# Performance work log

Hardware: AMD Instinct MI355X
Metric: run time of the kernel (lower is better)

Reference implementation:

```python
import jax, jax.numpy as jnp
import numpy as np

B, S, D_IN, D_OUT, H = 2, 2048, 1024, 1024, 16
HD = D_OUT // H  # head dim = 64


def setup_inputs() -> dict:
    key = jax.random.key(0)
    ks = jax.random.split(key, 9)
    s_in = 1.0 / np.sqrt(D_IN)
    s_out = 1.0 / np.sqrt(D_OUT)
    return {
        "X": jax.random.normal(ks[0], (B, S, D_IN), dtype=jnp.float32),
        "Wq": jax.random.uniform(ks[1], (D_OUT, D_IN), jnp.float32, -s_in, s_in),
        "bq": jax.random.uniform(ks[2], (D_OUT,), jnp.float32, -s_in, s_in),
        "Wk": jax.random.uniform(ks[3], (D_OUT, D_IN), jnp.float32, -s_in, s_in),
        "bk": jax.random.uniform(ks[4], (D_OUT,), jnp.float32, -s_in, s_in),
        "Wv": jax.random.uniform(ks[5], (D_OUT, D_IN), jnp.float32, -s_in, s_in),
        "bv": jax.random.uniform(ks[6], (D_OUT,), jnp.float32, -s_in, s_in),
        "Wo": jax.random.uniform(ks[7], (D_OUT, D_OUT), jnp.float32, -s_out, s_out),
        "bo": jax.random.uniform(ks[8], (D_OUT,), jnp.float32, -s_out, s_out),
    }


def reference(X, Wq, bq, Wk, bk, Wv, bv, Wo, bo):
    scale = jnp.asarray(HD ** 0.5, X.dtype)  # self.dim = sqrt(head_dim)
    q = X @ Wq.T + bq  # [B,S,D_OUT]
    k = X @ Wk.T + bk
    v = X @ Wv.T + bv
    # split heads: b s (h d) -> b h s d
    q = q.reshape(B, S, H, HD).transpose(0, 2, 1, 3)
    k = k.reshape(B, S, H, HD).transpose(0, 2, 1, 3)
    v = v.reshape(B, S, H, HD).transpose(0, 2, 1, 3)
    scores = jnp.einsum('bhsd,bhtd->bhst', q, k) / scale  # [B,H,S,S]
    causal = jnp.triu(jnp.ones((S, S), dtype=bool), k=1)
    scores = jnp.where(causal, -jnp.inf, scores)
    weights = jax.nn.softmax(scores, axis=-1)
    out = jnp.einsum('bhst,bhtd->bhsd', weights, v)  # [B,H,S,HD]
    out = out.transpose(0, 2, 1, 3).reshape(B, S, D_OUT)  # b h s d -> b s (h d)
    return out @ Wo.T + bo
```

## Files before the change

### kernel.cpp

```cpp
#include <hip/hip_runtime.h>
#include <hip/hip_bf16.h>

typedef __bf16 bf16_t;
typedef __bf16 bf16x8 __attribute__((ext_vector_type(8)));
typedef float  f32x4  __attribute__((ext_vector_type(4)));
typedef unsigned short ushort_t;

#define MFMA16(a, b, c) __builtin_amdgcn_mfma_f32_16x16x32_bf16((a), (b), (c), 0, 0, 0)
#define GLDS16(g, l) __builtin_amdgcn_global_load_lds( \
    (const __attribute__((address_space(1))) unsigned int*)(g), \
    (__attribute__((address_space(3))) unsigned int*)(l), 16, 0, 0)

#define WAITCNT_VM(n)  (0x0F70 | (n))
#define WAITCNT_LGKM0  0xC07F

#define QSCALE 0.18033688f

__global__ __launch_bounds__(256) void cvt_all(
    const void* __restrict__ X,  const void* __restrict__ W0, const void* __restrict__ W1,
    const void* __restrict__ W2, const void* __restrict__ W3,
    const void* __restrict__ c0, const void* __restrict__ c1,
    const void* __restrict__ c2, const void* __restrict__ c3,
    bf16_t* __restrict__ Xb, bf16_t* __restrict__ Wb, float* __restrict__ biasF,
    int* __restrict__ flag)
{
    const int tid  = threadIdx.x;
    const int lane = tid & 63;
    const ushort_t u = ((const ushort_t*)X)[2 * lane];
    const int e = (u >> 7) & 0xFF;
    const int f = (__ballot(e >= 0xA0) != 0ull) ? 1 : 0;

    const int bid = blockIdx.x;
    if (bid >= 4096) {
        if (bid == 4096 && tid == 0) *flag = f;
        const int idx = ((bid - 4096) * 256 + tid) * 8;
        const int w = idx >> 10, off = idx & 1023;
        const void* src = (w == 0) ? c0 : (w == 1) ? c1 : (w == 2) ? c2 : c3;
        #pragma unroll
        for (int r = 0; r < 8; ++r)
            biasF[idx + r] = f ? ((const float*)src)[off + r]
                               : (float)((const bf16_t*)src)[off + r];
        return;
    }

    const long long i = (long long)bid * 2048 + tid * 8;
    const void* src;
    bf16_t* dst;
    long long off;
    if (i < 4194304) { src = X; dst = Xb; off = i; }
    else {
        const int w = (int)((i - 4194304) >> 20);
        off = (i - 4194304) & 1048575;
        src = (w == 0) ? W0 : (w == 1) ? W1 : (w == 2) ? W2 : W3;
        dst = Wb + (size_t)w * 1048576;
    }
    if (f) {
        const float* s = (const float*)src + off;
        const float4 a = *(const float4*)(s);
        const float4 b = *(const float4*)(s + 4);
        bf16x8 o;
        o[0] = (bf16_t)a.x; o[1] = (bf16_t)a.y; o[2] = (bf16_t)a.z; o[3] = (bf16_t)a.w;
        o[4] = (bf16_t)b.x; o[5] = (bf16_t)b.y; o[6] = (bf16_t)b.z; o[7] = (bf16_t)b.w;
        *(bf16x8*)(dst + off) = o;
    } else {
        *(bf16x8*)(dst + off) = *(const bf16x8*)((const bf16_t*)src + off);
    }
}

template<int TM>
__global__ __launch_bounds__(256, 2) void gemm_nt(
    const bf16_t* __restrict__ A,
    const bf16_t* __restrict__ W0, const bf16_t* __restrict__ W1, const bf16_t* __restrict__ W2,
    const float* __restrict__ b0, const float* __restrict__ b1, const float* __restrict__ b2,
    void* __restrict__ C, int ldc, bf16_t* __restrict__ Vt, int fuse_vt,
    const int* __restrict__ flag, int is_out)
{
    constexpr int MI = TM / 32;
    constexpr int G  = (TM == 128) ? 4 : 3;
    __shared__ bf16_t Ash[3][TM * 32];
    __shared__ bf16_t Bsh[3][128 * 32];

    const int f32out = is_out ? *flag : 0;

    const int tid  = threadIdx.x;
    const int wid  = tid >> 6;
    const int lane = tid & 63;
    const int g    = lane >> 4;
    const int c    = lane & 15;

    const int m0  = blockIdx.x * TM;
    const int n0  = blockIdx.y * 128;
    const int mat = n0 >> 10;
    const bf16_t* W  = (mat == 0) ? W0 : (mat == 1) ? W1 : W2;
    const float*  bs = (mat == 0) ? b0 : (mat == 1) ? b1 : b2;
    const int nw = n0 & 1023;

    const int srow = lane >> 2;
    const int sblk = (lane & 3) ^ ((lane >> 3) & 3);
    const bf16_t* Ag = A + (size_t)(m0 + wid * (TM / 4) + srow) * 1024 + sblk * 8;
    const bf16_t* Wg = W + (size_t)(nw + wid * 32 + srow) * 1024 + sblk * 8;

    const int waveM = (wid >> 1) * (TM / 2);
    const int waveN = (wid & 1) * 64;

    f32x4 acc[MI][4] = {};
    const int fblk = (g ^ ((c >> 1) & 3)) * 8;

    auto stage = [&](int t, int buf) {
        const int k0 = t * 32;
        bf16_t* As = &Ash[buf][(wid * (TM / 4)) * 32];
        bf16_t* Bs = &Bsh[buf][(wid * 32) * 32];
        GLDS16(Ag + k0, As);
        if (TM == 128) GLDS16(Ag + (size_t)16 * 1024 + k0, As + 16 * 32);
        GLDS16(Wg + k0, Bs);
        GLDS16(Wg + (size_t)16 * 1024 + k0, Bs + 16 * 32);
    };

    stage(0, 0);
    stage(1, 1);

    #pragma unroll 3
    for (int k = 0; k < 32; ++k) {
        if (k < 30) {
            stage(k + 2, (k + 2) % 3);
            __builtin_amdgcn_s_waitcnt(WAITCNT_VM(2 * G));
        } else if (k == 30) {
            __builtin_amdgcn_s_waitcnt(WAITCNT_VM(G));
        } else {
            __builtin_amdgcn_s_waitcnt(WAITCNT_VM(0));
        }
        __builtin_amdgcn_s_barrier();
        asm volatile("" ::: "memory");

        const int cur = k % 3;
        bf16x8 af[MI], bfr[4];
        #pragma unroll
        for (int i = 0; i < MI; ++i)
            af[i] = *(const bf16x8*)(&Ash[cur][(waveM + i * 16 + c) * 32 + fblk]);
        #pragma unroll
        for (int j = 0; j < 4; ++j)
            bfr[j] = *(const bf16x8*)(&Bsh[cur][(waveN + j * 16 + c) * 32 + fblk]);
        #pragma unroll
        for (int i = 0; i < MI; ++i)
            #pragma unroll
            for (int j = 0; j < 4; ++j)
                acc[i][j] = MFMA16(af[i], bfr[j], acc[i][j]);

        asm volatile("" ::: "memory");
        __builtin_amdgcn_s_waitcnt(WAITCNT_LGKM0);
        __builtin_amdgcn_s_barrier();
    }

    if (fuse_vt && mat == 2) {
        #pragma unroll
        for (int j = 0; j < 4; ++j) {
            const int col  = n0 + waveN + j * 16 + c;
            const int hcol = col & 1023;
            const float bv = bs[hcol];
            const int h = hcol >> 6, d = hcol & 63;
            #pragma unroll
            for (int i = 0; i < MI; ++i) {
                const int row = m0 + waveM + i * 16 + g * 4;
                const int bb = row >> 11, s = row & 2047;
                bf16_t pk[4];
                #pragma unroll
                for (int r = 0; r < 4; ++r) pk[r] = (bf16_t)(acc[i][j][r] + bv);
                *(uint2*)(&Vt[(((size_t)bb * 16 + h) * 64 + d) * 2048 + s]) = *(uint2*)pk;
            }
        }
        return;
    }

    const float oscale = (fuse_vt && mat == 0) ? QSCALE : 1.0f;
    #pragma unroll
    for (int j = 0; j < 4; ++j) {
        const int col = n0 + waveN + j * 16 + c;
        const float bv = bs[col & 1023];
        #pragma unroll
        for (int i = 0; i < MI; ++i) {
            const int row = m0 + waveM + i * 16 + g * 4;
            #pragma unroll
            for (int r = 0; r < 4; ++r) {
                const float val = (acc[i][j][r] + bv) * oscale;
                const size_t idx = (size_t)(row + r) * ldc + col;
                if (f32out) ((float*)C)[idx] = val;
                else        ((bf16_t*)C)[idx] = (bf16_t)val;
            }
        }
    }
}

__global__ __launch_bounds__(256, 4) void attn_kernel(
    const bf16_t* __restrict__ QKV, const bf16_t* __restrict__ Vt,
    bf16_t* __restrict__ O)
{
    __shared__ bf16_t Ksh[64][72];
    __shared__ bf16_t Vsh[64][72];
    __shared__ bf16_t Psh[4][16][72];

    const int tid  = threadIdx.x;
    const int wid  = tid >> 6;
    const int lane = tid & 63;
    const int g    = lane >> 4;
    const int c    = lane & 15;

    const int bh = blockIdx.y;
    const int b  = bh >> 4, h = bh & 15;
    const int qt = (bh < 16) ? blockIdx.x : (31 - blockIdx.x);
    const int q0 = qt * 64;
    const int nt = qt + 1;

    bf16x8 aq[2];
    {
        const bf16_t* qp = QKV + (size_t)(b * 2048 + q0 + wid * 16 + c) * 3072 + h * 64;
        aq[0] = *(const bf16x8*)(qp + g * 8);
        aq[1] = *(const bf16x8*)(qp + 32 + g * 8);
    }

    float li[4] = {};
    f32x4 o[4]  = {};

    const int sr  = tid >> 2;
    const int sc0 = (tid & 3) * 16;
    const bf16_t* Kg = QKV + (size_t)(b * 2048 + sr) * 3072 + 1024 + h * 64 + sc0;
    const bf16_t* Vg = Vt + ((size_t)bh * 64 + sr) * 2048 + sc0;

    uint4 kr0 = *(const uint4*)(Kg);
    uint4 kr1 = *(const uint4*)(Kg + 8);
    uint4 vr0 = *(const uint4*)(Vg);
    uint4 vr1 = *(const uint4*)(Vg + 8);

    for (int jt = 0; jt < nt; ++jt) {
        *(uint4*)(&Ksh[sr][sc0])     = kr0;
        *(uint4*)(&Ksh[sr][sc0 + 8]) = kr1;
        *(uint4*)(&Vsh[sr][sc0])     = vr0;
        *(uint4*)(&Vsh[sr][sc0 + 8]) = vr1;
        __syncthreads();

        if (jt + 1 < nt) {
            const size_t ko = (size_t)(jt + 1) * 64 * 3072;
            kr0 = *(const uint4*)(Kg + ko);
            kr1 = *(const uint4*)(Kg + ko + 8);
            vr0 = *(const uint4*)(Vg + (jt + 1) * 64);
            vr1 = *(const uint4*)(Vg + (jt + 1) * 64 + 8);
        }

        f32x4 s[4] = {};
        #pragma unroll
        for (int n = 0; n < 4; ++n)
            #pragma unroll
            for (int kb = 0; kb < 2; ++kb) {
                const bf16x8 kf = *(const bf16x8*)(&Ksh[n * 16 + c][kb * 32 + g * 8]);
                s[n] = MFMA16(aq[kb], kf, s[n]);
            }

        if (jt == nt - 1) {
            const int j0 = jt * 64;
            const int qrow = q0 + wid * 16 + g * 4;
            #pragma unroll
            for (int n = 0; n < 4; ++n)
                #pragma unroll
                for (int r = 0; r < 4; ++r)
                    if (j0 + n * 16 + c > qrow + r) s[n][r] = -1e30f;
        }

        #pragma unroll
        for (int n = 0; n < 4; ++n)
            #pragma unroll
            for (int r = 0; r < 4; ++r) {
                const float p = __builtin_amdgcn_exp2f(s[n][r]);
                li[r] += p;
                Psh[wid][g * 4 + r][n * 16 + c] = (bf16_t)p;
            }
        __builtin_amdgcn_wave_barrier();

        #pragma unroll
        for (int kb = 0; kb < 2; ++kb) {
            const bf16x8 ap = *(const bf16x8*)(&Psh[wid][c][kb * 32 + g * 8]);
            #pragma unroll
            for (int d = 0; d < 4; ++d) {
                const bf16x8 vf = *(const bf16x8*)(&Vsh[d * 16 + c][kb * 32 + g * 8]);
                o[d] = MFMA16(ap, vf, o[d]);
            }
        }
        __syncthreads();
    }

    #pragma unroll
    for (int off = 1; off < 16; off <<= 1)
        #pragma unroll
        for (int r = 0; r < 4; ++r)
            li[r] += __shfl_xor(li[r], off, 64);

    const int orow = b * 2048 + q0 + wid * 16 + g * 4;
    #pragma unroll
    for (int r = 0; r < 4; ++r) {
        const float inv = 1.0f / li[r];
        #pragma unroll
        for (int d = 0; d < 4; ++d)
            O[(size_t)(orow + r) * 1024 + h * 64 + d * 16 + c] = (bf16_t)(o[d][r] * inv);
    }
}

extern "C" void kernel_launch(void* const* d_in, const int* in_sizes, int n_in,
                              void* d_out, int out_size, void* d_ws, size_t ws_size,
                              hipStream_t stream)
{
    const void* X  = d_in[0];
    const void* Wq = d_in[1];  const void* bq = d_in[2];
    const void* Wk = d_in[3];  const void* bk = d_in[4];
    const void* Wv = d_in[5];  const void* bv = d_in[6];
    const void* Wo = d_in[7];  const void* bo = d_in[8];

    int*    flag  = (int*)d_ws;
    float*  biasF = (float*)((char*)d_ws + 16);
    bf16_t* Xb    = (bf16_t*)((char*)d_ws + 16 + 16384);
    bf16_t* Wb    = Xb  + (size_t)4096 * 1024;
    bf16_t* QKV   = Wb  + (size_t)4 * 1024 * 1024;
    bf16_t* Vt    = QKV + (size_t)4096 * 3072;
    bf16_t* Ao    = Vt  + (size_t)4096 * 1024;

    const size_t MW = (size_t)1024 * 1024;

    cvt_all<<<4098, 256, 0, stream>>>(X, Wq, Wk, Wv, Wo, bq, bk, bv, bo,
                                      Xb, Wb, biasF, flag);

    gemm_nt<128><<<dim3(32, 24), 256, 0, stream>>>(
        Xb, Wb, Wb + MW, Wb + 2 * MW,
        biasF, biasF + 1024, biasF + 2048, QKV, 3072, Vt, 1, flag, 0);
    attn_kernel<<<dim3(32, 32), 256, 0, stream>>>(QKV, Vt, Ao);
    gemm_nt<64><<<dim3(64, 8), 256, 0, stream>>>(
        Ao, Wb + 3 * MW, Wb + 3 * MW, Wb + 3 * MW,
        biasF + 3072, biasF + 3072, biasF + 3072, d_out, 1024, (bf16_t*)nullptr, 0, flag, 1);
}
```

Baseline: 201.1 us.

## Add 256x256-tile, 8-wave QKV projection GEMM with 4-stage LDS pipeline

Replaces the 128x128-tile QKV projection GEMM with a new 512-thread kernel that computes 256x256 output tiles. It uses a four-buffer direct global-to-LDS prefetch ring with split half-phase MFMA blocks, barriers and raised wave priority. Larger tiles raise arithmetic intensity and cut global traffic per FLOP. The trade-offs are a grid of only 192 blocks on a 256-CU device, much more LDS (128KB) and a large register footprint. The epilogue keeps the Q scaling and the transposed V store.

```diff
diff --git a/kernel.cpp b/kernel.cpp
--- a/kernel.cpp
+++ b/kernel.cpp
@@ -13,6 +13,8 @@
 
 #define WAITCNT_VM(n)  (0x0F70 | (n))
 #define WAITCNT_LGKM0  0xC07F
+
+#define MEMFENCE asm volatile("" ::: "memory")
 
 #define QSCALE 0.18033688f
 
@@ -67,6 +69,141 @@
     }
 }
 
+__global__ __launch_bounds__(512, 2) void gemm256(
+    const bf16_t* __restrict__ A,
+    const bf16_t* __restrict__ W0, const bf16_t* __restrict__ W1, const bf16_t* __restrict__ W2,
+    const float* __restrict__ b0, const float* __restrict__ b1, const float* __restrict__ b2,
+    bf16_t* __restrict__ C, bf16_t* __restrict__ Vt)
+{
+    __shared__ bf16_t Ash[4][256 * 32];
+    __shared__ bf16_t Bsh[4][256 * 32];
+
+    const int tid  = threadIdx.x;
+    const int wid  = tid >> 6;
+    const int lane = tid & 63;
+    const int g    = lane >> 4;
+    const int c    = lane & 15;
+
+    const int m0  = blockIdx.x * 256;
+    const int n0  = blockIdx.y * 256;
+    const int mat = n0 >> 10;
+    const bf16_t* W  = (mat == 0) ? W0 : (mat == 1) ? W1 : W2;
+    const float*  bs = (mat == 0) ? b0 : (mat == 1) ? b1 : b2;
+    const int nw = n0 & 1023;
+
+    const int srow = lane >> 2;
+    const int sblk = (lane & 3) ^ ((lane >> 3) & 3);
+    const bf16_t* Ag = A + (size_t)(m0 + wid * 32 + srow) * 1024 + sblk * 8;
+    const bf16_t* Wg = W + (size_t)(nw + wid * 32 + srow) * 1024 + sblk * 8;
+
+    const int waveM = (wid >> 2) * 128;
+    const int waveN = (wid & 3) * 64;
+    const int fblk  = (g ^ ((c >> 1) & 3)) * 8;
+
+    f32x4 acc[8][4] = {};
+
+    auto stageA = [&](int H, int q) {
+        GLDS16(Ag + (size_t)(q * 16) * 1024 + H * 32, &Ash[H & 3][(wid * 32 + q * 16) * 32]);
+    };
+    auto stageB = [&](int H, int q) {
+        GLDS16(Wg + (size_t)(q * 16) * 1024 + H * 32, &Bsh[H & 3][(wid * 32 + q * 16) * 32]);
+    };
+
+    for (int H = 0; H < 3; ++H) {
+        stageA(H, 0); stageA(H, 1); stageB(H, 0); stageB(H, 1);
+    }
+    __builtin_amdgcn_s_waitcnt(WAITCNT_VM(8));
+    __builtin_amdgcn_s_barrier();
+    MEMFENCE;
+
+    #pragma unroll 1
+    for (int H = 0; H < 32; ++H) {
+        const int buf = H & 3;
+        const bf16_t* As = Ash[buf];
+        const bf16_t* Bs = Bsh[buf];
+        const bool pre = (H + 3 < 32);
+
+        bf16x8 bfr[4], af[4];
+        #pragma unroll
+        for (int j = 0; j < 4; ++j)
+            bfr[j] = *(const bf16x8*)(&Bs[(waveN + j * 16 + c) * 32 + fblk]);
+        #pragma unroll
+        for (int i = 0; i < 4; ++i)
+            af[i] = *(const bf16x8*)(&As[(waveM + i * 16 + c) * 32 + fblk]);
+        if (pre) { stageA(H + 3, 0); stageB(H + 3, 0); }
+        MEMFENCE;
+        __builtin_amdgcn_s_barrier();
+        __builtin_amdgcn_s_waitcnt(WAITCNT_LGKM0);
+        __builtin_amdgcn_sched_barrier(0);
+        __builtin_amdgcn_s_setprio(1);
+        #pragma unroll
+        for (int i = 0; i < 4; ++i)
+            #pragma unroll
+            for (int j = 0; j < 4; ++j)
+                acc[i][j] = MFMA16(af[i], bfr[j], acc[i][j]);
+        __builtin_amdgcn_s_setprio(0);
+        MEMFENCE;
+        __builtin_amdgcn_s_barrier();
+        MEMFENCE;
+
+        #pragma unroll
+        for (int i = 0; i < 4; ++i)
+            af[i] = *(const bf16x8*)(&As[(waveM + (i + 4) * 16 + c) * 32 + fblk]);
+        if (pre) { stageA(H + 3, 1); stageB(H + 3, 1); }
+        MEMFENCE;
+        __builtin_amdgcn_s_barrier();
+        __builtin_amdgcn_s_waitcnt(WAITCNT_LGKM0);
+        __builtin_amdgcn_sched_barrier(0);
+        __builtin_amdgcn_s_setprio(1);
+        #pragma unroll
+        for (int i = 0; i < 4; ++i)
+            #pragma unroll
+            for (int j = 0; j < 4; ++j)
+                acc[i + 4][j] = MFMA16(af[i], bfr[j], acc[i + 4][j]);
+        __builtin_amdgcn_s_setprio(0);
+        MEMFENCE;
+        if (H < 29)       __builtin_amdgcn_s_waitcnt(WAITCNT_VM(8));
+        else if (H == 29) __builtin_amdgcn_s_waitcnt(WAITCNT_VM(4));
+        else if (H == 30) __builtin_amdgcn_s_waitcnt(WAITCNT_VM(0));
+        __builtin_amdgcn_s_barrier();
+        MEMFENCE;
+    }
+
+    if (mat == 2) {
+        #pragma unroll
+        for (int j = 0; j < 4; ++j) {
+            const int col  = n0 + waveN + j * 16 + c;
+            const int hcol = col & 1023;
+            const float bv = bs[hcol];
+            const int h = hcol >> 6, d = hcol & 63;
+            #pragma unroll
+            for (int i = 0; i < 8; ++i) {
+                const int row = m0 + waveM + i * 16 + g * 4;
+                const int bb = row >> 11, s = row & 2047;
+                bf16_t pk[4];
+                #pragma unroll
+                for (int r = 0; r < 4; ++r) pk[r] = (bf16_t)(acc[i][j][r] + bv);
+                *(uint2*)(&Vt[(((size_t)bb * 16 + h) * 64 + d) * 2048 + s]) = *(uint2*)pk;
+            }
+        }
+        return;
+    }
+
+    const float os = (mat == 0) ? QSCALE : 1.0f;
+    #pragma unroll
+    for (int j = 0; j < 4; ++j) {
+        const int col = n0 + waveN + j * 16 + c;
+        const float bv = bs[col & 1023];
+        #pragma unroll
+        for (int i = 0; i < 8; ++i) {
+            const int row = m0 + waveM + i * 16 + g * 4;
+            #pragma unroll
+            for (int r = 0; r < 4; ++r)
+                C[(size_t)(row + r) * 3072 + col] = (bf16_t)((acc[i][j][r] + bv) * os);
+        }
+    }
+}
+
 template<int TM>
 __global__ __launch_bounds__(256, 2) void gemm_nt(
     const bf16_t* __restrict__ A,
@@ -325,9 +462,9 @@
     cvt_all<<<4098, 256, 0, stream>>>(X, Wq, Wk, Wv, Wo, bq, bk, bv, bo,
                                       Xb, Wb, biasF, flag);
 
-    gemm_nt<128><<<dim3(32, 24), 256, 0, stream>>>(
+    gemm256<<<dim3(16, 12), 512, 0, stream>>>(
         Xb, Wb, Wb + MW, Wb + 2 * MW,
-        biasF, biasF + 1024, biasF + 2048, QKV, 3072, Vt, 1, flag, 0);
+        biasF, biasF + 1024, biasF + 2048, QKV, Vt);
     attn_kernel<<<dim3(32, 32), 256, 0, stream>>>(QKV, Vt, Ao);
     gemm_nt<64><<<dim3(64, 8), 256, 0, stream>>>(
         Ao, Wb + 3 * MW, Wb + 3 * MW, Wb + 3 * MW,
```

New measurement: 202.1 us. No clear change (+0.5%).

## Switch GEMM to double-buffered LDS pipeline with raised occupancy and MFMA priority

Applied to the files above, without the earlier changes.

The projection GEMM moves from a three-stage LDS ring to two buffers. Each iteration now reads its fragments from LDS, issues the next tile's global-to-LDS loads, and then runs the MFMAs, so the loads can overlap the math while less shared memory is used per block. Launch bounds are raised to allow three blocks per CU. s_setprio is placed around the MFMA sections in both the GEMM and the attention kernel so matrix work gets scheduling priority. In exchange there is less prefetch depth: each iteration waits for its load to finish (vmcnt 0), which can expose memory latency, and the higher occupancy target may force register spills.

```diff
diff --git a/kernel.cpp b/kernel.cpp
--- a/kernel.cpp
+++ b/kernel.cpp
@@ -13,6 +13,8 @@
 
 #define WAITCNT_VM(n)  (0x0F70 | (n))
 #define WAITCNT_LGKM0  0xC07F
+
+#define MEMFENCE asm volatile("" ::: "memory")
 
 #define QSCALE 0.18033688f
 
@@ -68,7 +70,7 @@
 }
 
 template<int TM>
-__global__ __launch_bounds__(256, 2) void gemm_nt(
+__global__ __launch_bounds__(256, 3) void gemm_nt(
     const bf16_t* __restrict__ A,
     const bf16_t* __restrict__ W0, const bf16_t* __restrict__ W1, const bf16_t* __restrict__ W2,
     const float* __restrict__ b0, const float* __restrict__ b1, const float* __restrict__ b2,
@@ -76,9 +78,8 @@
     const int* __restrict__ flag, int is_out)
 {
     constexpr int MI = TM / 32;
-    constexpr int G  = (TM == 128) ? 4 : 3;
-    __shared__ bf16_t Ash[3][TM * 32];
-    __shared__ bf16_t Bsh[3][128 * 32];
+    __shared__ bf16_t Ash[2][TM * 32];
+    __shared__ bf16_t Bsh[2][128 * 32];
 
     const int f32out = is_out ? *flag : 0;
 
@@ -106,8 +107,9 @@
     f32x4 acc[MI][4] = {};
     const int fblk = (g ^ ((c >> 1) & 3)) * 8;
 
-    auto stage = [&](int t, int buf) {
+    auto stage = [&](int t) {
         const int k0 = t * 32;
+        const int buf = t & 1;
         bf16_t* As = &Ash[buf][(wid * (TM / 4)) * 32];
         bf16_t* Bs = &Bsh[buf][(wid * 32) * 32];
         GLDS16(Ag + k0, As);
@@ -116,23 +118,14 @@
         GLDS16(Wg + (size_t)16 * 1024 + k0, Bs + 16 * 32);
     };
 
-    stage(0, 0);
-    stage(1, 1);
-
-    #pragma unroll 3
+    stage(0);
+    __builtin_amdgcn_s_waitcnt(WAITCNT_VM(0));
+    __builtin_amdgcn_s_barrier();
+    MEMFENCE;
+
+    #pragma unroll 2
     for (int k = 0; k < 32; ++k) {
-        if (k < 30) {
-            stage(k + 2, (k + 2) % 3);
-            __builtin_amdgcn_s_waitcnt(WAITCNT_VM(2 * G));
-        } else if (k == 30) {
-            __builtin_amdgcn_s_waitcnt(WAITCNT_VM(G));
-        } else {
-            __builtin_amdgcn_s_waitcnt(WAITCNT_VM(0));
-        }
-        __builtin_amdgcn_s_barrier();
-        asm volatile("" ::: "memory");
-
-        const int cur = k % 3;
+        const int cur = k & 1;
         bf16x8 af[MI], bfr[4];
         #pragma unroll
         for (int i = 0; i < MI; ++i)
@@ -140,15 +133,22 @@
         #pragma unroll
         for (int j = 0; j < 4; ++j)
             bfr[j] = *(const bf16x8*)(&Bsh[cur][(waveN + j * 16 + c) * 32 + fblk]);
+
+        if (k < 31) stage(k + 1);
+
+        __builtin_amdgcn_s_setprio(1);
         #pragma unroll
         for (int i = 0; i < MI; ++i)
             #pragma unroll
             for (int j = 0; j < 4; ++j)
                 acc[i][j] = MFMA16(af[i], bfr[j], acc[i][j]);
-
-        asm volatile("" ::: "memory");
+        __builtin_amdgcn_s_setprio(0);
+
+        MEMFENCE;
         __builtin_amdgcn_s_waitcnt(WAITCNT_LGKM0);
+        if (k < 31) __builtin_amdgcn_s_waitcnt(WAITCNT_VM(0));
         __builtin_amdgcn_s_barrier();
+        MEMFENCE;
     }
 
     if (fuse_vt && mat == 2) {
@@ -246,6 +246,7 @@
         }
 
         f32x4 s[4] = {};
+        __builtin_amdgcn_s_setprio(1);
         #pragma unroll
         for (int n = 0; n < 4; ++n)
             #pragma unroll
@@ -253,6 +254,7 @@
                 const bf16x8 kf = *(const bf16x8*)(&Ksh[n * 16 + c][kb * 32 + g * 8]);
                 s[n] = MFMA16(aq[kb], kf, s[n]);
             }
+        __builtin_amdgcn_s_setprio(0);
 
         if (jt == nt - 1) {
             const int j0 = jt * 64;
@@ -274,6 +276,7 @@
             }
         __builtin_amdgcn_wave_barrier();
 
+        __builtin_amdgcn_s_setprio(1);
         #pragma unroll
         for (int kb = 0; kb < 2; ++kb) {
             const bf16x8 ap = *(const bf16x8*)(&Psh[wid][c][kb * 32 + g * 8]);
@@ -283,6 +286,7 @@
                 o[d] = MFMA16(ap, vf, o[d]);
             }
         }
+        __builtin_amdgcn_s_setprio(0);
         __syncthreads();
     }
 
```

After: 200.6 us. No clear change (-0.3%).
